# Kernel tuning notes

Hardware: AMD Instinct MI355X
Metric: run time of the kernel (lower is better)

Reference implementation:

```python
import jax, jax.numpy as jnp
import numpy as np

ALPHA = 0.3        # Keras LeakyReLU default negative_slope
NUM_STEPS = 16     # fixed-step Dormand-Prince (see notes)
DEPTH = 10
HID = 1024
LOOK = 30
BATCH = 16384


def _leaky(x):
    return jnp.where(x > 0, x, ALPHA * x)


def _mlp(y, W1, b1, W2, b2, W3, b3):
    # drift f(y): 30 -> 1024 -> 1024 -> 30, autonomous (t unused)
    h = _leaky(jnp.dot(y, W1) + b1)
    h = _leaky(jnp.dot(h, W2) + b2)
    return jnp.dot(h, W3) + b3


def _dopri5_step(y, h, params):
    f = lambda z: _mlp(z, *params)
    k1 = f(y)
    k2 = f(y + h * (1.0 / 5.0) * k1)
    k3 = f(y + h * (3.0 / 40.0 * k1 + 9.0 / 40.0 * k2))
    k4 = f(y + h * (44.0 / 45.0 * k1 - 56.0 / 15.0 * k2 + 32.0 / 9.0 * k3))
    k5 = f(y + h * (19372.0 / 6561.0 * k1 - 25360.0 / 2187.0 * k2
                    + 64448.0 / 6561.0 * k3 - 212.0 / 729.0 * k4))
    k6 = f(y + h * (9017.0 / 3168.0 * k1 - 355.0 / 33.0 * k2
                    + 46732.0 / 5247.0 * k3 + 49.0 / 176.0 * k4
                    - 5103.0 / 18656.0 * k5))
    # 5th-order solution (b row of the Dormand-Prince tableau)
    return y + h * (35.0 / 384.0 * k1 + 500.0 / 1113.0 * k3
                    + 125.0 / 192.0 * k4 - 2187.0 / 6784.0 * k5
                    + 11.0 / 84.0 * k6)


def _solve_block(y0, params):
    # integrate dy/dt = f(y) from t=0 to t=1 with fixed step h
    h = 1.0 / NUM_STEPS
    def step(y, _):
        return _dopri5_step(y, h, params), None
    y, _ = jax.lax.scan(step, y0, None, length=NUM_STEPS)
    return y


def setup_inputs() -> dict:
    key = jax.random.key(0)
    ks = jax.random.split(key, 9)
    y0 = jax.random.normal(ks[0], (BATCH, 1, LOOK), dtype=jnp.float32)
    s1 = 1.0 / np.sqrt(LOOK)
    s2 = 1.0 / np.sqrt(HID)
    W1 = jax.random.normal(ks[1], (DEPTH, LOOK, HID), dtype=jnp.float32) * s1
    b1 = jnp.zeros((DEPTH, HID), dtype=jnp.float32)
    W2 = jax.random.normal(ks[2], (DEPTH, HID, HID), dtype=jnp.float32) * s2
    b2 = jnp.zeros((DEPTH, HID), dtype=jnp.float32)
    W3 = jax.random.normal(ks[3], (DEPTH, HID, LOOK), dtype=jnp.float32) * s2
    b3 = jnp.zeros((DEPTH, LOOK), dtype=jnp.float32)
    Wf = jax.random.normal(ks[4], (LOOK, 1), dtype=jnp.float32) * s1
    bf = jnp.zeros((1,), dtype=jnp.float32)
    return {"y0": y0, "W1": W1, "b1": b1, "W2": W2, "b2": b2,
            "W3": W3, "b3": b3, "Wf": Wf, "bf": bf}


def reference(y0, W1, b1, W2, b2, W3, b3, Wf, bf):
    # sequentially apply DEPTH ODE blocks, each with its own drift MLP
    def block(y, p):
        return _solve_block(y, p), None
    y, _ = jax.lax.scan(block, y0, (W1, b1, W2, b2, W3, b3))
    # final readout Dense(output_dim=1)
    return jnp.dot(y, Wf) + bf  # (B, 1, 1)
```

## Files before the change

### kernel.cpp

```cpp
#include <hip/hip_runtime.h>

#define BATCH 16384
#define LOOK 30
#define HID 1024
#define DEPTH 10
#define NSTEPS 16
#define ALPHA 0.3f

typedef short bf16x8 __attribute__((ext_vector_type(8)));
typedef float f32x4 __attribute__((ext_vector_type(4)));

__device__ __forceinline__ float leaky(float x) { return x > 0.f ? x : ALPHA * x; }

__device__ __forceinline__ unsigned short f2bf(float x) {
  unsigned u = __builtin_bit_cast(unsigned, x);
  unsigned r = u + 0x7FFFu + ((u >> 16) & 1u);
  return (unsigned short)(r >> 16);
}
__device__ __forceinline__ float bf2f(unsigned short b) {
  return __builtin_bit_cast(float, (unsigned)b << 16);
}

#define GLD_LDS16(g, l)                                        \
  __builtin_amdgcn_global_load_lds(                            \
      (const __attribute__((address_space(1))) void*)(g),      \
      (__attribute__((address_space(3))) void*)(l), 16, 0, 0)

__global__ __launch_bounds__(256) void k_w2split(const float* __restrict__ W2d,
                                                 short* __restrict__ W2Th,
                                                 short* __restrict__ W2Tl) {
  __shared__ float t[64][65];
  const int kb = blockIdx.x * 64;
  const int nb = blockIdx.y * 64;
  for (int i = threadIdx.x; i < 4096; i += 256) {
    int r = i >> 6, c = i & 63;
    t[r][c] = W2d[(size_t)(kb + r) * HID + nb + c];
  }
  __syncthreads();
  for (int i = threadIdx.x; i < 4096; i += 256) {
    int r = i >> 6, c = i & 63;
    float v = t[c][r];
    unsigned short hi = f2bf(v);
    unsigned short lo = f2bf(v - bf2f(hi));
    W2Th[(size_t)(nb + r) * HID + kb + c] = (short)hi;
    W2Tl[(size_t)(nb + r) * HID + kb + c] = (short)lo;
  }
}

__global__ __launch_bounds__(256) void k_w1t(const float* __restrict__ W1d,
                                             short* __restrict__ W1Th,
                                             short* __restrict__ W1Tl) {
  const int idx = blockIdx.x * 256 + threadIdx.x;
  if (idx >= 1024 * 32) return;
  const int n = idx >> 5, k = idx & 31;
  float v = (k < LOOK) ? W1d[(size_t)k * HID + n] : 0.f;
  unsigned short hi = f2bf(v);
  unsigned short lo = f2bf(v - bf2f(hi));
  W1Th[idx] = (short)hi;
  W1Tl[idx] = (short)lo;
}

__global__ __launch_bounds__(256) void k_w3t(const float* __restrict__ W3d,
                                             short* __restrict__ W3Th,
                                             short* __restrict__ W3Tl) {
  const int idx = blockIdx.x * 256 + threadIdx.x;
  if (idx >= 32 * 1024) return;
  const int n = idx >> 10, k = idx & 1023;
  float v = (n < LOOK) ? W3d[(size_t)k * LOOK + n] : 0.f;
  unsigned short hi = f2bf(v);
  unsigned short lo = f2bf(v - bf2f(hi));
  W3Th[idx] = (short)hi;
  W3Tl[idx] = (short)lo;
}

__global__ __launch_bounds__(256) void k_zinit(const float* __restrict__ y0,
                                               short* __restrict__ zh,
                                               short* __restrict__ zl) {
  const int idx = blockIdx.x * 256 + threadIdx.x;
  if (idx >= BATCH * 32) return;
  const int r = idx >> 5, c = idx & 31;
  float v = (c < LOOK) ? y0[(size_t)r * LOOK + c] : 0.f;
  unsigned short hi = f2bf(v);
  unsigned short lo = f2bf(v - bf2f(hi));
  zh[idx] = (short)hi;
  zl[idx] = (short)lo;
}

__global__ __launch_bounds__(512, 2) void k_l1(
    const short* __restrict__ zh, const short* __restrict__ zl,
    const short* __restrict__ W1Th, const short* __restrict__ W1Tl,
    const float* __restrict__ b1d, short* __restrict__ H1h,
    short* __restrict__ H1l) {
  __shared__ short za[2][128 * 32];
  const int tid = threadIdx.x, lane = tid & 63, wave = tid >> 6;
  const int row0 = blockIdx.x * 128;
  const int n0 = blockIdx.y * 256;
  const int wm = wave >> 2, wn = wave & 3;
  const int r15 = lane & 15;
  const int bk = (lane >> 4) * 8;

  bf16x8 bh[4], bl[4];
#pragma unroll
  for (int nj = 0; nj < 4; ++nj) {
    const size_t bo = (size_t)(n0 + wn * 64 + nj * 16 + r15) * 32 + bk;
    bh[nj] = *(const bf16x8*)&W1Th[bo];
    bl[nj] = *(const bf16x8*)&W1Tl[bo];
  }

  GLD_LDS16((const char*)(zh + (size_t)row0 * 32) + tid * 16, &za[0][tid * 8]);
  GLD_LDS16((const char*)(zl + (size_t)row0 * 32) + tid * 16, &za[1][tid * 8]);
  __syncthreads();

  bf16x8 ah[4], al[4];
#pragma unroll
  for (int mi = 0; mi < 4; ++mi) {
    const int ao = (wm * 64 + mi * 16 + r15) * 32 + bk;
    ah[mi] = *(const bf16x8*)&za[0][ao];
    al[mi] = *(const bf16x8*)&za[1][ao];
  }

  f32x4 acc[4][4];
#pragma unroll
  for (int i = 0; i < 4; ++i)
#pragma unroll
    for (int j = 0; j < 4; ++j) acc[i][j] = (f32x4){0.f, 0.f, 0.f, 0.f};

#pragma unroll
  for (int mi = 0; mi < 4; ++mi)
#pragma unroll
    for (int nj = 0; nj < 4; ++nj) {
      acc[mi][nj] = __builtin_amdgcn_mfma_f32_16x16x32_bf16(ah[mi], bh[nj],
                                                            acc[mi][nj], 0, 0, 0);
      acc[mi][nj] = __builtin_amdgcn_mfma_f32_16x16x32_bf16(ah[mi], bl[nj],
                                                            acc[mi][nj], 0, 0, 0);
      acc[mi][nj] = __builtin_amdgcn_mfma_f32_16x16x32_bf16(al[mi], bh[nj],
                                                            acc[mi][nj], 0, 0, 0);
    }

  const int crow = (lane >> 4) * 4;
#pragma unroll
  for (int nj = 0; nj < 4; ++nj) {
    const int col = n0 + wn * 64 + nj * 16 + r15;
    const float bias = b1d[col];
#pragma unroll
    for (int mi = 0; mi < 4; ++mi) {
      const int rb = row0 + wm * 64 + mi * 16 + crow;
#pragma unroll
      for (int r = 0; r < 4; ++r) {
        float v = leaky(acc[mi][nj][r] + bias);
        unsigned short hi = f2bf(v);
        unsigned short lo = f2bf(v - bf2f(hi));
        const size_t o = (size_t)(rb + r) * HID + col;
        H1h[o] = (short)hi;
        H1l[o] = (short)lo;
      }
    }
  }
}

__global__ __launch_bounds__(512, 2) void k_mid(
    const short* __restrict__ H1h, const short* __restrict__ H1l,
    const short* __restrict__ W2Th, const short* __restrict__ W2Tl,
    const float* __restrict__ b2d, short* __restrict__ H2h,
    short* __restrict__ H2l) {
  __shared__ char lds[131072];

  const int tid = threadIdx.x;
  const int lane = tid & 63;
  const int wave = tid >> 6;

  const int bid = blockIdx.x;
  const int wg = (bid & 7) * 32 + (bid >> 3);
  const int mb = wg >> 2, nb = wg & 3;
  const int row0 = mb * 256;
  const int n0 = nb * 256;
  const int wm = wave >> 2;
  const int wnb = wave & 3;

  const int l3 = lane >> 3;
  const int l7 = lane & 7;
  const int s = l7 ^ l3;
  const char* hsrc;
  const char* lsrc;
  int rbase;
  if (wave < 4) {
    hsrc = (const char*)H1h;
    lsrc = (const char*)H1l;
    rbase = row0;
  } else {
    hsrc = (const char*)W2Th;
    lsrc = (const char*)W2Tl;
    rbase = n0;
  }
  const char* srcB[8];
#pragma unroll
  for (int i = 0; i < 8; ++i) {
    const int c = wave * 8 + i;
    const int rloc = (c & 31) * 8 + l3;
    const char* base = (s < 4) ? hsrc : lsrc;
    srcB[i] = base + (size_t)(rbase + rloc) * 2048 + (size_t)(s & 3) * 16;
  }
  const int dchunk0 = wave * 8 * 1024;

  int offA0, offA1, offB0, offB1;
  {
    const int r15 = lane & 15;
    const int kq = lane >> 4;
    const int pa0 = ((0 * 4 + kq) ^ l7) * 16;
    const int pa1 = ((1 * 4 + kq) ^ l7) * 16;
    offA0 = (wm * 128 + r15) * 128 + pa0;
    offA1 = (wm * 128 + r15) * 128 + pa1;
    offB0 = 32768 + (wnb * 64 + r15) * 128 + pa0;
    offB1 = 32768 + (wnb * 64 + r15) * 128 + pa1;
  }

  f32x4 acc[8][4];
#pragma unroll
  for (int i = 0; i < 8; ++i)
#pragma unroll
    for (int j = 0; j < 4; ++j) acc[i][j] = (f32x4){0.f, 0.f, 0.f, 0.f};

#define STAGE(buf, kb)                                                   \
  {                                                                      \
    _Pragma("unroll") for (int i = 0; i < 8; ++i) {                      \
      GLD_LDS16(srcB[i] + (kb), &lds[(buf)*65536 + dchunk0 + i * 1024]); \
    }                                                                    \
  }

  STAGE(0, 0);
  __syncthreads();

  int cur = 0;
  for (int t = 0; t < 32; ++t) {
    if (t < 31) STAGE(cur ^ 1, (t + 1) * 64);

    const char* buf = &lds[cur * 65536];
    bf16x8 bh[4], bl[4];
#pragma unroll
    for (int nj = 0; nj < 4; ++nj) {
      bh[nj] = *(const bf16x8*)(buf + offB0 + nj * 2048);
      bl[nj] = *(const bf16x8*)(buf + offB1 + nj * 2048);
    }
#pragma unroll
    for (int mi = 0; mi < 8; ++mi) {
      bf16x8 ah = *(const bf16x8*)(buf + offA0 + mi * 2048);
      bf16x8 al = *(const bf16x8*)(buf + offA1 + mi * 2048);
#pragma unroll
      for (int nj = 0; nj < 4; ++nj) {
        acc[mi][nj] =
            __builtin_amdgcn_mfma_f32_16x16x32_bf16(ah, bh[nj], acc[mi][nj], 0, 0, 0);
        acc[mi][nj] =
            __builtin_amdgcn_mfma_f32_16x16x32_bf16(ah, bl[nj], acc[mi][nj], 0, 0, 0);
        acc[mi][nj] =
            __builtin_amdgcn_mfma_f32_16x16x32_bf16(al, bh[nj], acc[mi][nj], 0, 0, 0);
      }
    }
    __syncthreads();
    cur ^= 1;
  }
#undef STAGE

  const int crow = (lane >> 4) * 4;
  const int ccol = lane & 15;
#pragma unroll
  for (int nj = 0; nj < 4; ++nj) {
    const int col = n0 + wnb * 64 + nj * 16 + ccol;
    const float bv = b2d[col];
#pragma unroll
    for (int mi = 0; mi < 8; ++mi) {
      const int rb = row0 + wm * 128 + mi * 16 + crow;
#pragma unroll
      for (int r = 0; r < 4; ++r) {
        float v = leaky(acc[mi][nj][r] + bv);
        unsigned short hi = f2bf(v);
        unsigned short lo = f2bf(v - bf2f(hi));
        const size_t o = (size_t)(rb + r) * HID + col;
        H2h[o] = (short)hi;
        H2l[o] = (short)lo;
      }
    }
  }
}

__global__ __launch_bounds__(256, 4) void k_l3(
    const short* __restrict__ H2h, const short* __restrict__ H2l,
    const short* __restrict__ W3Th, const short* __restrict__ W3Tl,
    const float* __restrict__ b3d, float* __restrict__ kout,
    const float* __restrict__ K0, const float* __restrict__ K1,
    const float* __restrict__ K2, const float* __restrict__ K3,
    const float* __restrict__ K4, float* __restrict__ y,
    short* __restrict__ zh, short* __restrict__ zl, int combine, float p1,
    float p2, float p3, float p4, float p5, float pc, float hb1, float hb2,
    float hb3, float hb4, float hb5, float hb6) {
  __shared__ short lds[2][4096];

  const int tid = threadIdx.x, lane = tid & 63, wave = tid >> 6;
  const int row0 = blockIdx.x * 32;
  const int wm = wave & 1, wn = wave >> 1;

  const int half = tid >> 7;
  const int idx = tid & 127;
  const int srow = idx >> 2;
  const int sd = idx & 3;
  const int slog = sd ^ ((srow >> 1) & 3);
  const short* Asrc = half ? H2l : H2h;
  const short* Bsrc = half ? W3Tl : W3Th;
  const char* aSrc = (const char*)(Asrc + (size_t)(row0 + srow) * HID) + slog * 16;
  const char* bSrc = (const char*)(Bsrc + (size_t)srow * HID) + slog * 16;
  short* aDst0 = &lds[0][half * 1024 + idx * 8];
  short* bDst0 = &lds[0][2048 + half * 1024 + idx * 8];
  short* aDst1 = &lds[1][half * 1024 + idx * 8];
  short* bDst1 = &lds[1][2048 + half * 1024 + idx * 8];

  const int r15 = lane & 15;
  const int kc = lane >> 4;
  const int aRow = wm * 16 + r15;
  const int bRow = wn * 16 + r15;
  const int aOff = aRow * 32 + (kc ^ ((aRow >> 1) & 3)) * 8;
  const int bOff = 2048 + bRow * 32 + (kc ^ ((bRow >> 1) & 3)) * 8;

  f32x4 acc = (f32x4){0.f, 0.f, 0.f, 0.f};

#define STAGE3(ad, bd, kb)          \
  {                                 \
    GLD_LDS16(aSrc + (kb), (ad));   \
    GLD_LDS16(bSrc + (kb), (bd));   \
  }

  STAGE3(aDst0, bDst0, 0);
  __syncthreads();

  for (int t = 0; t < 32; ++t) {
    const int cur = t & 1;
    if (t < 31) {
      if (cur == 0) STAGE3(aDst1, bDst1, (t + 1) * 64)
      else STAGE3(aDst0, bDst0, (t + 1) * 64)
    }
    const short* buf = lds[cur];
    bf16x8 ah = *(const bf16x8*)(buf + aOff);
    bf16x8 al = *(const bf16x8*)(buf + 1024 + aOff);
    bf16x8 bh = *(const bf16x8*)(buf + bOff);
    bf16x8 bl = *(const bf16x8*)(buf + 1024 + bOff);
    acc = __builtin_amdgcn_mfma_f32_16x16x32_bf16(ah, bh, acc, 0, 0, 0);
    acc = __builtin_amdgcn_mfma_f32_16x16x32_bf16(ah, bl, acc, 0, 0, 0);
    acc = __builtin_amdgcn_mfma_f32_16x16x32_bf16(al, bh, acc, 0, 0, 0);
    __syncthreads();
  }
#undef STAGE3

  const int c = wn * 16 + r15;
  const int rb = row0 + wm * 16 + (lane >> 4) * 4;
  const float bias = (c < LOOK) ? b3d[c] : 0.f;
#pragma unroll
  for (int r = 0; r < 4; ++r) {
    const int row = rb + r;
    const float kv = acc[r] + bias;
    float zv = 0.f;
    if (c < LOOK) {
      const size_t id = (size_t)row * LOOK + c;
      const float yv = y[id];
      if (combine) {
        float yn = yv + hb1 * K0[id] + hb2 * K1[id] + hb3 * K2[id] +
                   hb4 * K3[id] + hb5 * K4[id] + hb6 * kv;
        y[id] = yn;
        zv = yn;
      } else {
        kout[id] = kv;
        zv = yv + pc * kv;
        if (p1 != 0.f) zv += p1 * K0[id];
        if (p2 != 0.f) zv += p2 * K1[id];
        if (p3 != 0.f) zv += p3 * K2[id];
        if (p4 != 0.f) zv += p4 * K3[id];
        if (p5 != 0.f) zv += p5 * K4[id];
      }
    }
    unsigned short hi = f2bf(zv);
    unsigned short lo = f2bf(zv - bf2f(hi));
    const size_t zo = (size_t)row * 32 + c;
    zh[zo] = (short)hi;
    zl[zo] = (short)lo;
  }
}

__global__ __launch_bounds__(256) void k_readout(const float* __restrict__ y,
                                                 const float* __restrict__ Wf,
                                                 const float* __restrict__ bf,
                                                 float* __restrict__ out) {
  const int r = blockIdx.x * blockDim.x + threadIdx.x;
  if (r >= BATCH) return;
  float acc = bf[0];
#pragma unroll
  for (int c = 0; c < LOOK; ++c) acc += y[(size_t)r * LOOK + c] * Wf[c];
  out[r] = acc;
}

extern "C" void kernel_launch(void* const* d_in, const int* in_sizes, int n_in,
                              void* d_out, int out_size, void* d_ws,
                              size_t ws_size, hipStream_t stream) {
  const float* y0 = (const float*)d_in[0];
  const float* W1 = (const float*)d_in[1];
  const float* b1 = (const float*)d_in[2];
  const float* W2 = (const float*)d_in[3];
  const float* b2 = (const float*)d_in[4];
  const float* W3 = (const float*)d_in[5];
  const float* b3 = (const float*)d_in[6];
  const float* Wf = (const float*)d_in[7];
  const float* bf = (const float*)d_in[8];
  float* out = (float*)d_out;

  const size_t NY = (size_t)BATCH * LOOK;
  float* f = (float*)d_ws;
  float* y = f;
  float* kk[5];
  for (int i = 0; i < 5; ++i) kk[i] = f + NY * (1 + i);
  char* p = (char*)(f + NY * 6);
  short* zh = (short*)p; p += (size_t)BATCH * 32 * 2;
  short* zl = (short*)p; p += (size_t)BATCH * 32 * 2;
  short* H1h = (short*)p; p += (size_t)BATCH * HID * 2;
  short* H1l = (short*)p; p += (size_t)BATCH * HID * 2;
  short* H2h = (short*)p; p += (size_t)BATCH * HID * 2;
  short* H2l = (short*)p; p += (size_t)BATCH * HID * 2;
  short* W2Th = (short*)p; p += (size_t)HID * HID * 2;
  short* W2Tl = (short*)p; p += (size_t)HID * HID * 2;
  short* W1Th = (short*)p; p += (size_t)HID * 32 * 2;
  short* W1Tl = (short*)p; p += (size_t)HID * 32 * 2;
  short* W3Th = (short*)p; p += (size_t)32 * HID * 2;
  short* W3Tl = (short*)p;

  hipMemcpyAsync(y, y0, NY * sizeof(float), hipMemcpyDeviceToDevice, stream);
  k_zinit<<<dim3(BATCH * 32 / 256), 256, 0, stream>>>(y0, zh, zl);

  const double hh = 1.0 / 16.0;
  static const double A[6][5] = {
      {0, 0, 0, 0, 0},
      {1.0 / 5, 0, 0, 0, 0},
      {3.0 / 40, 9.0 / 40, 0, 0, 0},
      {44.0 / 45, -56.0 / 15, 32.0 / 9, 0, 0},
      {19372.0 / 6561, -25360.0 / 2187, 64448.0 / 6561, -212.0 / 729, 0},
      {9017.0 / 3168, -355.0 / 33, 46732.0 / 5247, 49.0 / 176,
       -5103.0 / 18656},
  };
  static const double Bb[6] = {35.0 / 384,  0,              500.0 / 1113,
                               125.0 / 192, -2187.0 / 6784, 11.0 / 84};

  const float hb1 = (float)(hh * Bb[0]);
  const float hb2 = (float)(hh * Bb[1]);
  const float hb3 = (float)(hh * Bb[2]);
  const float hb4 = (float)(hh * Bb[3]);
  const float hb5 = (float)(hh * Bb[4]);
  const float hb6 = (float)(hh * Bb[5]);

  for (int d = 0; d < DEPTH; ++d) {
    const float* W1d = W1 + (size_t)d * LOOK * HID;
    const float* b1d = b1 + (size_t)d * HID;
    const float* W2d = W2 + (size_t)d * HID * HID;
    const float* b2d = b2 + (size_t)d * HID;
    const float* W3d = W3 + (size_t)d * HID * LOOK;
    const float* b3d = b3 + (size_t)d * LOOK;

    k_w2split<<<dim3(16, 16), 256, 0, stream>>>(W2d, W2Th, W2Tl);
    k_w1t<<<dim3(128), 256, 0, stream>>>(W1d, W1Th, W1Tl);
    k_w3t<<<dim3(128), 256, 0, stream>>>(W3d, W3Th, W3Tl);

    for (int s = 0; s < NSTEPS; ++s) {
      for (int st = 0; st < 6; ++st) {
        float pv[5] = {0.f, 0.f, 0.f, 0.f, 0.f};
        float pc = 0.f;
        if (st < 5) {
          for (int jj = 0; jj < 5; ++jj)
            if (jj < st) pv[jj] = (float)(hh * A[st + 1][jj]);
          pc = (float)(hh * A[st + 1][st]);
        }
        k_l1<<<dim3(BATCH / 128, HID / 256), 512, 0, stream>>>(
            zh, zl, W1Th, W1Tl, b1d, H1h, H1l);
        k_mid<<<dim3(256), 512, 0, stream>>>(H1h, H1l, W2Th, W2Tl, b2d, H2h,
                                             H2l);
        const int comb = (st == 5) ? 1 : 0;
        float* kout = (st < 5) ? kk[st] : kk[0];
        k_l3<<<dim3(BATCH / 32), 256, 0, stream>>>(
            H2h, H2l, W3Th, W3Tl, b3d, kout, kk[0], kk[1], kk[2], kk[3],
            kk[4], y, zh, zl, comb, pv[0], pv[1], pv[2], pv[3], pv[4], pc,
            hb1, hb2, hb3, hb4, hb5, hb6);
      }
    }
  }

  k_readout<<<dim3(BATCH / 256), 256, 0, stream>>>(y, Wf, bf, out);
}
```

Baseline: 137.6 ms.

## Fuse first MLP layer into second-layer GEMM, computing H1 tiles on the fly

Removes the separate layer-1 kernel and its H1 hi/lo round trip through global memory. Each block now computes the 256x64 slice of H1 for every k-step with MFMA from the z inputs and W1, applies bias and leaky, splits the result into bf16 hi/lo and writes it straight into LDS for the W2 GEMM. Only the W2 tiles are double-buffered through global-to-LDS loads, synchronised with manual waitcnt and barriers plus setprio around the MFMA loop. The price is layer-1 work recomputed by each of the four N-blocks and extra per-iteration ALU and LDS-store work on the critical path.

Result: slower. 145.5 ms (+5.7%).

```diff
diff --git a/kernel.cpp b/kernel.cpp
--- a/kernel.cpp
+++ b/kernel.cpp
@@ -86,84 +86,13 @@
   zl[idx] = (short)lo;
 }
 
-__global__ __launch_bounds__(512, 2) void k_l1(
+__global__ __launch_bounds__(512, 2) void k_mid(
     const short* __restrict__ zh, const short* __restrict__ zl,
     const short* __restrict__ W1Th, const short* __restrict__ W1Tl,
-    const float* __restrict__ b1d, short* __restrict__ H1h,
-    short* __restrict__ H1l) {
-  __shared__ short za[2][128 * 32];
-  const int tid = threadIdx.x, lane = tid & 63, wave = tid >> 6;
-  const int row0 = blockIdx.x * 128;
-  const int n0 = blockIdx.y * 256;
-  const int wm = wave >> 2, wn = wave & 3;
-  const int r15 = lane & 15;
-  const int bk = (lane >> 4) * 8;
-
-  bf16x8 bh[4], bl[4];
-#pragma unroll
-  for (int nj = 0; nj < 4; ++nj) {
-    const size_t bo = (size_t)(n0 + wn * 64 + nj * 16 + r15) * 32 + bk;
-    bh[nj] = *(const bf16x8*)&W1Th[bo];
-    bl[nj] = *(const bf16x8*)&W1Tl[bo];
-  }
-
-  GLD_LDS16((const char*)(zh + (size_t)row0 * 32) + tid * 16, &za[0][tid * 8]);
-  GLD_LDS16((const char*)(zl + (size_t)row0 * 32) + tid * 16, &za[1][tid * 8]);
-  __syncthreads();
-
-  bf16x8 ah[4], al[4];
-#pragma unroll
-  for (int mi = 0; mi < 4; ++mi) {
-    const int ao = (wm * 64 + mi * 16 + r15) * 32 + bk;
-    ah[mi] = *(const bf16x8*)&za[0][ao];
-    al[mi] = *(const bf16x8*)&za[1][ao];
-  }
-
-  f32x4 acc[4][4];
-#pragma unroll
-  for (int i = 0; i < 4; ++i)
-#pragma unroll
-    for (int j = 0; j < 4; ++j) acc[i][j] = (f32x4){0.f, 0.f, 0.f, 0.f};
-
-#pragma unroll
-  for (int mi = 0; mi < 4; ++mi)
-#pragma unroll
-    for (int nj = 0; nj < 4; ++nj) {
-      acc[mi][nj] = __builtin_amdgcn_mfma_f32_16x16x32_bf16(ah[mi], bh[nj],
-                                                            acc[mi][nj], 0, 0, 0);
-      acc[mi][nj] = __builtin_amdgcn_mfma_f32_16x16x32_bf16(ah[mi], bl[nj],
-                                                            acc[mi][nj], 0, 0, 0);
-      acc[mi][nj] = __builtin_amdgcn_mfma_f32_16x16x32_bf16(al[mi], bh[nj],
-                                                            acc[mi][nj], 0, 0, 0);
-    }
-
-  const int crow = (lane >> 4) * 4;
-#pragma unroll
-  for (int nj = 0; nj < 4; ++nj) {
-    const int col = n0 + wn * 64 + nj * 16 + r15;
-    const float bias = b1d[col];
-#pragma unroll
-    for (int mi = 0; mi < 4; ++mi) {
-      const int rb = row0 + wm * 64 + mi * 16 + crow;
-#pragma unroll
-      for (int r = 0; r < 4; ++r) {
-        float v = leaky(acc[mi][nj][r] + bias);
-        unsigned short hi = f2bf(v);
-        unsigned short lo = f2bf(v - bf2f(hi));
-        const size_t o = (size_t)(rb + r) * HID + col;
-        H1h[o] = (short)hi;
-        H1l[o] = (short)lo;
-      }
-    }
-  }
-}
-
-__global__ __launch_bounds__(512, 2) void k_mid(
-    const short* __restrict__ H1h, const short* __restrict__ H1l,
-    const short* __restrict__ W2Th, const short* __restrict__ W2Tl,
-    const float* __restrict__ b2d, short* __restrict__ H2h,
-    short* __restrict__ H2l) {
-  __shared__ char lds[131072];
+    const float* __restrict__ b1d, const short* __restrict__ W2Th,
+    const short* __restrict__ W2Tl, const float* __restrict__ b2d,
+    short* __restrict__ H2h, short* __restrict__ H2l) {
+  __shared__ char lds[98304];
 
   const int tid = threadIdx.x;
   const int lane = tid & 63;
@@ -176,43 +105,34 @@
   const int n0 = nb * 256;
   const int wm = wave >> 2;
   const int wnb = wave & 3;
-
+  const int r15 = lane & 15;
+  const int kq = lane >> 4;
+  const int l7 = lane & 7;
   const int l3 = lane >> 3;
-  const int l7 = lane & 7;
-  const int s = l7 ^ l3;
-  const char* hsrc;
-  const char* lsrc;
-  int rbase;
-  if (wave < 4) {
-    hsrc = (const char*)H1h;
-    lsrc = (const char*)H1l;
-    rbase = row0;
-  } else {
-    hsrc = (const char*)W2Th;
-    lsrc = (const char*)W2Tl;
-    rbase = n0;
-  }
-  const char* srcB[8];
-#pragma unroll
-  for (int i = 0; i < 8; ++i) {
-    const int c = wave * 8 + i;
-    const int rloc = (c & 31) * 8 + l3;
-    const char* base = (s < 4) ? hsrc : lsrc;
-    srcB[i] = base + (size_t)(rbase + rloc) * 2048 + (size_t)(s & 3) * 16;
-  }
-  const int dchunk0 = wave * 8 * 1024;
-
-  int offA0, offA1, offB0, offB1;
+
+  const char* srcB[4];
   {
-    const int r15 = lane & 15;
-    const int kq = lane >> 4;
-    const int pa0 = ((0 * 4 + kq) ^ l7) * 16;
-    const int pa1 = ((1 * 4 + kq) ^ l7) * 16;
-    offA0 = (wm * 128 + r15) * 128 + pa0;
-    offA1 = (wm * 128 + r15) * 128 + pa1;
-    offB0 = 32768 + (wnb * 64 + r15) * 128 + pa0;
-    offB1 = 32768 + (wnb * 64 + r15) * 128 + pa1;
-  }
+    const int s = l7 ^ l3;
+    const char* base = (s < 4) ? (const char*)W2Th : (const char*)W2Tl;
+#pragma unroll
+    for (int i = 0; i < 4; ++i) {
+      const int c = wave * 4 + i;
+      srcB[i] = base + (size_t)(n0 + c * 8 + l3) * 2048 + (size_t)(s & 3) * 16;
+    }
+  }
+
+  bf16x8 zf[2][2];
+#pragma unroll
+  for (int rt = 0; rt < 2; ++rt) {
+    const size_t zo = (size_t)(row0 + wave * 32 + rt * 16 + r15) * 32 + kq * 8;
+    zf[rt][0] = *(const bf16x8*)&zh[zo];
+    zf[rt][1] = *(const bf16x8*)&zl[zo];
+  }
+
+  const int offA0 = (wm * 128 + r15) * 128 + ((0 + kq) ^ l7) * 16;
+  const int offA1 = (wm * 128 + r15) * 128 + ((4 + kq) ^ l7) * 16;
+  const int offB0 = (wnb * 64 + r15) * 128 + ((0 + kq) ^ l7) * 16;
+  const int offB1 = (wnb * 64 + r15) * 128 + ((4 + kq) ^ l7) * 16;
 
   f32x4 acc[8][4];
 #pragma unroll
@@ -220,31 +140,87 @@
 #pragma unroll
     for (int j = 0; j < 4; ++j) acc[i][j] = (f32x4){0.f, 0.f, 0.f, 0.f};
 
-#define STAGE(buf, kb)                                                   \
-  {                                                                      \
-    _Pragma("unroll") for (int i = 0; i < 8; ++i) {                      \
-      GLD_LDS16(srcB[i] + (kb), &lds[(buf)*65536 + dchunk0 + i * 1024]); \
-    }                                                                    \
-  }
-
-  STAGE(0, 0);
-  __syncthreads();
-
-  int cur = 0;
+#pragma unroll
+  for (int i = 0; i < 4; ++i)
+    GLD_LDS16(srcB[i], &lds[32768 + (wave * 4 + i) * 1024]);
+
   for (int t = 0; t < 32; ++t) {
-    if (t < 31) STAGE(cur ^ 1, (t + 1) * 64);
-
-    const char* buf = &lds[cur * 65536];
+    bf16x8 w1[2][2];
+    float4 b1v[2];
+#pragma unroll
+    for (int kt = 0; kt < 2; ++kt) {
+      const size_t wo = (size_t)(t * 32 + kt * 16 + r15) * 32 + kq * 8;
+      w1[kt][0] = *(const bf16x8*)&W1Th[wo];
+      w1[kt][1] = *(const bf16x8*)&W1Tl[wo];
+      b1v[kt] = *(const float4*)&b1d[t * 32 + kt * 16 + kq * 4];
+    }
+
+    if (t < 31) {
+      const int kb = (t + 1) * 64;
+      char* dst = &lds[32768 + ((t + 1) & 1) * 32768];
+#pragma unroll
+      for (int i = 0; i < 4; ++i)
+        GLD_LDS16(srcB[i] + kb, dst + (wave * 4 + i) * 1024);
+    }
+
+    f32x4 h1a[2][2];
+#pragma unroll
+    for (int kt = 0; kt < 2; ++kt)
+#pragma unroll
+      for (int rt = 0; rt < 2; ++rt) {
+        f32x4 a = (f32x4){0.f, 0.f, 0.f, 0.f};
+        a = __builtin_amdgcn_mfma_f32_16x16x32_bf16(w1[kt][0], zf[rt][0], a, 0, 0, 0);
+        a = __builtin_amdgcn_mfma_f32_16x16x32_bf16(w1[kt][1], zf[rt][0], a, 0, 0, 0);
+        a = __builtin_amdgcn_mfma_f32_16x16x32_bf16(w1[kt][0], zf[rt][1], a, 0, 0, 0);
+        h1a[kt][rt] = a;
+      }
+
+#pragma unroll
+    for (int kt = 0; kt < 2; ++kt)
+#pragma unroll
+      for (int rt = 0; rt < 2; ++rt) {
+        unsigned short hs[4], ls[4];
+#pragma unroll
+        for (int r = 0; r < 4; ++r) {
+          float v = leaky(h1a[kt][rt][r] + b1v[kt][r]);
+          hs[r] = f2bf(v);
+          ls[r] = f2bf(v - bf2f(hs[r]));
+        }
+        const int row = wave * 32 + rt * 16 + r15;
+        const int bb = row * 128 + (kq & 1) * 8;
+        const int so = kt * 2 + (kq >> 1);
+        const int sh = ((0 + so) ^ l7) * 16;
+        const int sl = ((4 + so) ^ l7) * 16;
+        uint2 hp, lp;
+        hp.x = (unsigned)hs[0] | ((unsigned)hs[1] << 16);
+        hp.y = (unsigned)hs[2] | ((unsigned)hs[3] << 16);
+        lp.x = (unsigned)ls[0] | ((unsigned)ls[1] << 16);
+        lp.y = (unsigned)ls[2] | ((unsigned)ls[3] << 16);
+        *(uint2*)&lds[bb + sh] = hp;
+        *(uint2*)&lds[bb + sl] = lp;
+      }
+
+    __builtin_amdgcn_sched_barrier(0);
+    if (t < 31) {
+      asm volatile("s_waitcnt vmcnt(4) lgkmcnt(0)" ::: "memory");
+    } else {
+      asm volatile("s_waitcnt vmcnt(0) lgkmcnt(0)" ::: "memory");
+    }
+    __builtin_amdgcn_sched_barrier(0);
+    __builtin_amdgcn_s_barrier();
+
+    const char* bufB = &lds[32768 + (t & 1) * 32768];
     bf16x8 bh[4], bl[4];
 #pragma unroll
     for (int nj = 0; nj < 4; ++nj) {
-      bh[nj] = *(const bf16x8*)(buf + offB0 + nj * 2048);
-      bl[nj] = *(const bf16x8*)(buf + offB1 + nj * 2048);
-    }
+      bh[nj] = *(const bf16x8*)(bufB + offB0 + nj * 2048);
+      bl[nj] = *(const bf16x8*)(bufB + offB1 + nj * 2048);
+    }
+    __builtin_amdgcn_s_setprio(1);
 #pragma unroll
     for (int mi = 0; mi < 8; ++mi) {
-      bf16x8 ah = *(const bf16x8*)(buf + offA0 + mi * 2048);
-      bf16x8 al = *(const bf16x8*)(buf + offA1 + mi * 2048);
+      bf16x8 ah = *(const bf16x8*)(lds + offA0 + mi * 2048);
+      bf16x8 al = *(const bf16x8*)(lds + offA1 + mi * 2048);
 #pragma unroll
       for (int nj = 0; nj < 4; ++nj) {
         acc[mi][nj] =
@@ -255,16 +231,16 @@
             __builtin_amdgcn_mfma_f32_16x16x32_bf16(al, bh[nj], acc[mi][nj], 0, 0, 0);
       }
     }
-    __syncthreads();
-    cur ^= 1;
-  }
-#undef STAGE
+    __builtin_amdgcn_s_setprio(0);
+
+    __builtin_amdgcn_sched_barrier(0);
+    __builtin_amdgcn_s_barrier();
+  }
 
   const int crow = (lane >> 4) * 4;
-  const int ccol = lane & 15;
 #pragma unroll
   for (int nj = 0; nj < 4; ++nj) {
-    const int col = n0 + wnb * 64 + nj * 16 + ccol;
+    const int col = n0 + wnb * 64 + nj * 16 + r15;
     const float bv = b2d[col];
 #pragma unroll
     for (int mi = 0; mi < 8; ++mi) {
@@ -416,8 +392,6 @@
   char* p = (char*)(f + NY * 6);
   short* zh = (short*)p; p += (size_t)BATCH * 32 * 2;
   short* zl = (short*)p; p += (size_t)BATCH * 32 * 2;
-  short* H1h = (short*)p; p += (size_t)BATCH * HID * 2;
-  short* H1l = (short*)p; p += (size_t)BATCH * HID * 2;
   short* H2h = (short*)p; p += (size_t)BATCH * HID * 2;
   short* H2l = (short*)p; p += (size_t)BATCH * HID * 2;
   short* W2Th = (short*)p; p += (size_t)HID * HID * 2;
@@ -471,10 +445,8 @@
             if (jj < st) pv[jj] = (float)(hh * A[st + 1][jj]);
           pc = (float)(hh * A[st + 1][st]);
         }
-        k_l1<<<dim3(BATCH / 128, HID / 256), 512, 0, stream>>>(
-            zh, zl, W1Th, W1Tl, b1d, H1h, H1l);
-        k_mid<<<dim3(256), 512, 0, stream>>>(H1h, H1l, W2Th, W2Tl, b2d, H2h,
-                                             H2l);
+        k_mid<<<dim3(256), 512, 0, stream>>>(zh, zl, W1Th, W1Tl, b1d, W2Th,
+                                             W2Tl, b2d, H2h, H2l);
         const int comb = (st == 5) ? 1 : 0;
         float* kout = (st < 5) ? kk[st] : kk[0];
         k_l3<<<dim3(BATCH / 32), 256, 0, stream>>>(
```

## Hand-schedule MFMA pipeline in k_mid and deepen k_l3 prefetch ring

Applied to the files above, without the earlier changes.

In k_mid, LDS fragment reads are split into two halves, each followed by its MFMA block. Explicit sched_barriers, waitcnts and s_setprio raise priority around the MFMA clusters, and the next tile's global-to-LDS loads are issued after the first fragment reads. In k_l3, the double buffer becomes a 4-slot ring with prefetch distance 2 and partial vmcnt waits, so more loads stay in flight. The aim is better overlap of memory and MFMA, at the cost of fragile manual scheduling and extra LDS in k_l3.

Result: slower. 140.8 ms (+2.3%).

```diff
diff --git a/kernel.cpp b/kernel.cpp
--- a/kernel.cpp
+++ b/kernel.cpp
@@ -25,6 +25,24 @@
   __builtin_amdgcn_global_load_lds(                            \
       (const __attribute__((address_space(1))) void*)(g),      \
       (__attribute__((address_space(3))) void*)(l), 16, 0, 0)
+
+#define SBAR()                               \
+  {                                          \
+    __builtin_amdgcn_sched_barrier(0);       \
+    __builtin_amdgcn_s_barrier();            \
+  }
+#define WAIT_LGKM0()                                          \
+  {                                                           \
+    __builtin_amdgcn_sched_barrier(0);                        \
+    asm volatile("s_waitcnt lgkmcnt(0)" ::: "memory");        \
+    __builtin_amdgcn_sched_barrier(0);                        \
+  }
+#define WAIT_VM(n)                                            \
+  {                                                           \
+    __builtin_amdgcn_sched_barrier(0);                        \
+    asm volatile("s_waitcnt vmcnt(" #n ")" ::: "memory");     \
+    __builtin_amdgcn_sched_barrier(0);                        \
+  }
 
 __global__ __launch_bounds__(256) void k_w2split(const float* __restrict__ W2d,
                                                  short* __restrict__ W2Th,
@@ -176,43 +194,40 @@
   const int n0 = nb * 256;
   const int wm = wave >> 2;
   const int wnb = wave & 3;
-
+  const int r15 = lane & 15;
+  const int kq = lane >> 4;
+  const int l7 = lane & 7;
   const int l3 = lane >> 3;
-  const int l7 = lane & 7;
-  const int s = l7 ^ l3;
-  const char* hsrc;
-  const char* lsrc;
-  int rbase;
-  if (wave < 4) {
-    hsrc = (const char*)H1h;
-    lsrc = (const char*)H1l;
-    rbase = row0;
-  } else {
-    hsrc = (const char*)W2Th;
-    lsrc = (const char*)W2Tl;
-    rbase = n0;
-  }
+
   const char* srcB[8];
-#pragma unroll
-  for (int i = 0; i < 8; ++i) {
-    const int c = wave * 8 + i;
-    const int rloc = (c & 31) * 8 + l3;
+  {
+    const int s = l7 ^ l3;
+    const char* hsrc;
+    const char* lsrc;
+    int rbase;
+    if (wave < 4) {
+      hsrc = (const char*)H1h;
+      lsrc = (const char*)H1l;
+      rbase = row0;
+    } else {
+      hsrc = (const char*)W2Th;
+      lsrc = (const char*)W2Tl;
+      rbase = n0;
+    }
     const char* base = (s < 4) ? hsrc : lsrc;
-    srcB[i] = base + (size_t)(rbase + rloc) * 2048 + (size_t)(s & 3) * 16;
-  }
-  const int dchunk0 = wave * 8 * 1024;
-
-  int offA0, offA1, offB0, offB1;
-  {
-    const int r15 = lane & 15;
-    const int kq = lane >> 4;
-    const int pa0 = ((0 * 4 + kq) ^ l7) * 16;
-    const int pa1 = ((1 * 4 + kq) ^ l7) * 16;
-    offA0 = (wm * 128 + r15) * 128 + pa0;
-    offA1 = (wm * 128 + r15) * 128 + pa1;
-    offB0 = 32768 + (wnb * 64 + r15) * 128 + pa0;
-    offB1 = 32768 + (wnb * 64 + r15) * 128 + pa1;
-  }
+#pragma unroll
+    for (int i = 0; i < 8; ++i) {
+      const int c = wave * 8 + i;
+      const int rloc = (c & 31) * 8 + l3;
+      srcB[i] = base + (size_t)(rbase + rloc) * 2048 + (size_t)(s & 3) * 16;
+    }
+  }
+  const int dchunk0 = wave * 8192;
+
+  const int offA0 = (wm * 128 + r15) * 128 + ((0 + kq) ^ l7) * 16;
+  const int offA1 = (wm * 128 + r15) * 128 + ((4 + kq) ^ l7) * 16;
+  const int offB0 = 32768 + (wnb * 64 + r15) * 128 + ((0 + kq) ^ l7) * 16;
+  const int offB1 = 32768 + (wnb * 64 + r15) * 128 + ((4 + kq) ^ l7) * 16;
 
   f32x4 acc[8][4];
 #pragma unroll
@@ -220,61 +235,96 @@
 #pragma unroll
     for (int j = 0; j < 4; ++j) acc[i][j] = (f32x4){0.f, 0.f, 0.f, 0.f};
 
-#define STAGE(buf, kb)                                                   \
-  {                                                                      \
-    _Pragma("unroll") for (int i = 0; i < 8; ++i) {                      \
-      GLD_LDS16(srcB[i] + (kb), &lds[(buf)*65536 + dchunk0 + i * 1024]); \
-    }                                                                    \
-  }
-
-  STAGE(0, 0);
-  __syncthreads();
-
-  int cur = 0;
-  for (int t = 0; t < 32; ++t) {
-    if (t < 31) STAGE(cur ^ 1, (t + 1) * 64);
-
-    const char* buf = &lds[cur * 65536];
-    bf16x8 bh[4], bl[4];
+#define STAGE4(bufbase, kb, h)                                             \
+  {                                                                        \
+    _Pragma("unroll") for (int i_ = 0; i_ < 4; ++i_) {                     \
+      GLD_LDS16(srcB[(h)*4 + i_] + (kb),                                   \
+                &lds[(bufbase) + dchunk0 + ((h)*4 + i_) * 1024]);          \
+    }                                                                      \
+  }
+
+  STAGE4(0, 0, 0);
+  STAGE4(0, 0, 1);
+  WAIT_VM(0);
+  SBAR();
+
+  for (int tt = 0; tt < 32; ++tt) {
+    const int rb = (tt & 1) * 65536;
+    const int wb = ((tt + 1) & 1) * 65536;
+    const int kb = (tt + 1) * 64;
+
+    bf16x8 bh[4], bl[4], ah[4], al[4];
+
 #pragma unroll
     for (int nj = 0; nj < 4; ++nj) {
-      bh[nj] = *(const bf16x8*)(buf + offB0 + nj * 2048);
-      bl[nj] = *(const bf16x8*)(buf + offB1 + nj * 2048);
-    }
+      bh[nj] = *(const bf16x8*)(lds + rb + offB0 + nj * 2048);
+      bl[nj] = *(const bf16x8*)(lds + rb + offB1 + nj * 2048);
+    }
+#pragma unroll
+    for (int q = 0; q < 4; ++q) {
+      ah[q] = *(const bf16x8*)(lds + rb + offA0 + q * 2048);
+      al[q] = *(const bf16x8*)(lds + rb + offA1 + q * 2048);
+    }
+    if (tt < 31) {
+      STAGE4(wb, kb, 0);
+      STAGE4(wb, kb, 1);
+    }
+    SBAR();
+    WAIT_LGKM0();
+    __builtin_amdgcn_s_setprio(1);
+#pragma unroll
+    for (int q = 0; q < 4; ++q)
+#pragma unroll
+      for (int nj = 0; nj < 4; ++nj) {
+        acc[q][nj] =
+            __builtin_amdgcn_mfma_f32_16x16x32_bf16(ah[q], bh[nj], acc[q][nj], 0, 0, 0);
+        acc[q][nj] =
+            __builtin_amdgcn_mfma_f32_16x16x32_bf16(ah[q], bl[nj], acc[q][nj], 0, 0, 0);
+        acc[q][nj] =
+            __builtin_amdgcn_mfma_f32_16x16x32_bf16(al[q], bh[nj], acc[q][nj], 0, 0, 0);
+      }
+    __builtin_amdgcn_s_setprio(0);
+    SBAR();
+
+#pragma unroll
+    for (int q = 0; q < 4; ++q) {
+      ah[q] = *(const bf16x8*)(lds + rb + offA0 + (4 + q) * 2048);
+      al[q] = *(const bf16x8*)(lds + rb + offA1 + (4 + q) * 2048);
+    }
+    SBAR();
+    WAIT_LGKM0();
+    __builtin_amdgcn_s_setprio(1);
+#pragma unroll
+    for (int q = 0; q < 4; ++q)
+#pragma unroll
+      for (int nj = 0; nj < 4; ++nj) {
+        acc[4 + q][nj] =
+            __builtin_amdgcn_mfma_f32_16x16x32_bf16(ah[q], bh[nj], acc[4 + q][nj], 0, 0, 0);
+        acc[4 + q][nj] =
+            __builtin_amdgcn_mfma_f32_16x16x32_bf16(ah[q], bl[nj], acc[4 + q][nj], 0, 0, 0);
+        acc[4 + q][nj] =
+            __builtin_amdgcn_mfma_f32_16x16x32_bf16(al[q], bh[nj], acc[4 + q][nj], 0, 0, 0);
+      }
+    __builtin_amdgcn_s_setprio(0);
+    WAIT_VM(0);
+    SBAR();
+  }
+#undef STAGE4
+
+  const int crow = (lane >> 4) * 4;
+#pragma unroll
+  for (int nj = 0; nj < 4; ++nj) {
+    const int col = n0 + wnb * 64 + nj * 16 + r15;
+    const float bv = b2d[col];
 #pragma unroll
     for (int mi = 0; mi < 8; ++mi) {
-      bf16x8 ah = *(const bf16x8*)(buf + offA0 + mi * 2048);
-      bf16x8 al = *(const bf16x8*)(buf + offA1 + mi * 2048);
-#pragma unroll
-      for (int nj = 0; nj < 4; ++nj) {
-        acc[mi][nj] =
-            __builtin_amdgcn_mfma_f32_16x16x32_bf16(ah, bh[nj], acc[mi][nj], 0, 0, 0);
-        acc[mi][nj] =
-            __builtin_amdgcn_mfma_f32_16x16x32_bf16(ah, bl[nj], acc[mi][nj], 0, 0, 0);
-        acc[mi][nj] =
-            __builtin_amdgcn_mfma_f32_16x16x32_bf16(al, bh[nj], acc[mi][nj], 0, 0, 0);
-      }
-    }
-    __syncthreads();
-    cur ^= 1;
-  }
-#undef STAGE
-
-  const int crow = (lane >> 4) * 4;
-  const int ccol = lane & 15;
-#pragma unroll
-  for (int nj = 0; nj < 4; ++nj) {
-    const int col = n0 + wnb * 64 + nj * 16 + ccol;
-    const float bv = b2d[col];
-#pragma unroll
-    for (int mi = 0; mi < 8; ++mi) {
-      const int rb = row0 + wm * 128 + mi * 16 + crow;
+      const int rbrow = row0 + wm * 128 + mi * 16 + crow;
 #pragma unroll
       for (int r = 0; r < 4; ++r) {
         float v = leaky(acc[mi][nj][r] + bv);
         unsigned short hi = f2bf(v);
         unsigned short lo = f2bf(v - bf2f(hi));
-        const size_t o = (size_t)(rb + r) * HID + col;
+        const size_t o = (size_t)(rbrow + r) * HID + col;
         H2h[o] = (short)hi;
         H2l[o] = (short)lo;
       }
@@ -292,7 +342,7 @@
     short* __restrict__ zh, short* __restrict__ zl, int combine, float p1,
     float p2, float p3, float p4, float p5, float pc, float hb1, float hb2,
     float hb3, float hb4, float hb5, float hb6) {
-  __shared__ short lds[2][4096];
+  __shared__ short lds[4][4096];
 
   const int tid = threadIdx.x, lane = tid & 63, wave = tid >> 6;
   const int row0 = blockIdx.x * 32;
@@ -307,10 +357,13 @@
   const short* Bsrc = half ? W3Tl : W3Th;
   const char* aSrc = (const char*)(Asrc + (size_t)(row0 + srow) * HID) + slog * 16;
   const char* bSrc = (const char*)(Bsrc + (size_t)srow * HID) + slog * 16;
-  short* aDst0 = &lds[0][half * 1024 + idx * 8];
-  short* bDst0 = &lds[0][2048 + half * 1024 + idx * 8];
-  short* aDst1 = &lds[1][half * 1024 + idx * 8];
-  short* bDst1 = &lds[1][2048 + half * 1024 + idx * 8];
+  short* aDst[4];
+  short* bDst[4];
+#pragma unroll
+  for (int s = 0; s < 4; ++s) {
+    aDst[s] = &lds[s][half * 1024 + idx * 8];
+    bDst[s] = &lds[s][2048 + half * 1024 + idx * 8];
+  }
 
   const int r15 = lane & 15;
   const int kc = lane >> 4;
@@ -321,22 +374,20 @@
 
   f32x4 acc = (f32x4){0.f, 0.f, 0.f, 0.f};
 
-#define STAGE3(ad, bd, kb)          \
-  {                                 \
-    GLD_LDS16(aSrc + (kb), (ad));   \
-    GLD_LDS16(bSrc + (kb), (bd));   \
-  }
-
-  STAGE3(aDst0, bDst0, 0);
-  __syncthreads();
+#define STG(s, kb)                        \
+  {                                       \
+    GLD_LDS16(aSrc + (kb), aDst[s]);      \
+    GLD_LDS16(bSrc + (kb), bDst[s]);      \
+  }
+
+  STG(0, 0);
+  STG(1, 64);
+  WAIT_VM(2);
+  SBAR();
 
   for (int t = 0; t < 32; ++t) {
-    const int cur = t & 1;
-    if (t < 31) {
-      if (cur == 0) STAGE3(aDst1, bDst1, (t + 1) * 64)
-      else STAGE3(aDst0, bDst0, (t + 1) * 64)
-    }
-    const short* buf = lds[cur];
+    if (t + 2 < 32) STG((t + 2) & 3, (t + 2) * 64);
+    const short* buf = lds[t & 3];
     bf16x8 ah = *(const bf16x8*)(buf + aOff);
     bf16x8 al = *(const bf16x8*)(buf + 1024 + aOff);
     bf16x8 bh = *(const bf16x8*)(buf + bOff);
@@ -344,16 +395,21 @@
     acc = __builtin_amdgcn_mfma_f32_16x16x32_bf16(ah, bh, acc, 0, 0, 0);
     acc = __builtin_amdgcn_mfma_f32_16x16x32_bf16(ah, bl, acc, 0, 0, 0);
     acc = __builtin_amdgcn_mfma_f32_16x16x32_bf16(al, bh, acc, 0, 0, 0);
-    __syncthreads();
-  }
-#undef STAGE3
+    if (t + 2 < 32) {
+      WAIT_VM(2);
+    } else {
+      WAIT_VM(0);
+    }
+    SBAR();
+  }
+#undef STG
 
   const int c = wn * 16 + r15;
-  const int rb = row0 + wm * 16 + (lane >> 4) * 4;
+  const int rbrow = row0 + wm * 16 + (lane >> 4) * 4;
   const float bias = (c < LOOK) ? b3d[c] : 0.f;
 #pragma unroll
   for (int r = 0; r < 4; ++r) {
-    const int row = rb + r;
+    const int row = rbrow + r;
     const float kv = acc[r] + bias;
     float zv = 0.f;
     if (c < LOOK) {
```

## Load W2 operand directly from global and quad-buffer activations with one barrier per step

Applied to the files above, without the earlier changes.

The hidden-layer GEMM kernel stops staging the weight (B) tile through LDS. Each wave now reads its B fragments directly from global memory. Only the activation (A) tile is staged, through a 4-deep LDS ring buffer with a prefetch distance of two iterations. Manual vmcnt waits with a single barrier per k-step replace the two __syncthreads, and s_setprio raises priority during the MFMA block. This halves LDS traffic and sync cost, but B is now reloaded per wave from global/L2 and those loads are exposed latency inside the loop.

New measurement: 163.6 ms. 18.9% more time.

```diff
diff --git a/kernel.cpp b/kernel.cpp
--- a/kernel.cpp
+++ b/kernel.cpp
@@ -176,42 +176,33 @@
   const int n0 = nb * 256;
   const int wm = wave >> 2;
   const int wnb = wave & 3;
-
+  const int r15 = lane & 15;
+  const int kq = lane >> 4;
+  const int l7 = lane & 7;
   const int l3 = lane >> 3;
-  const int l7 = lane & 7;
-  const int s = l7 ^ l3;
-  const char* hsrc;
-  const char* lsrc;
-  int rbase;
-  if (wave < 4) {
-    hsrc = (const char*)H1h;
-    lsrc = (const char*)H1l;
-    rbase = row0;
-  } else {
-    hsrc = (const char*)W2Th;
-    lsrc = (const char*)W2Tl;
-    rbase = n0;
-  }
-  const char* srcB[8];
-#pragma unroll
-  for (int i = 0; i < 8; ++i) {
-    const int c = wave * 8 + i;
-    const int rloc = (c & 31) * 8 + l3;
-    const char* base = (s < 4) ? hsrc : lsrc;
-    srcB[i] = base + (size_t)(rbase + rloc) * 2048 + (size_t)(s & 3) * 16;
-  }
-  const int dchunk0 = wave * 8 * 1024;
-
-  int offA0, offA1, offB0, offB1;
+
+  const char* srcA[4];
   {
-    const int r15 = lane & 15;
-    const int kq = lane >> 4;
-    const int pa0 = ((0 * 4 + kq) ^ l7) * 16;
-    const int pa1 = ((1 * 4 + kq) ^ l7) * 16;
-    offA0 = (wm * 128 + r15) * 128 + pa0;
-    offA1 = (wm * 128 + r15) * 128 + pa1;
-    offB0 = 32768 + (wnb * 64 + r15) * 128 + pa0;
-    offB1 = 32768 + (wnb * 64 + r15) * 128 + pa1;
+    const int s = l7 ^ l3;
+    const char* base = (s < 4) ? (const char*)H1h : (const char*)H1l;
+#pragma unroll
+    for (int i = 0; i < 4; ++i) {
+      const int c = wave * 4 + i;
+      srcA[i] = base + (size_t)(row0 + c * 8 + l3) * 2048 + (size_t)(s & 3) * 16;
+    }
+  }
+  const int dchunk0 = wave * 4096;
+
+  const int offA0 = (wm * 128 + r15) * 128 + ((0 + kq) ^ l7) * 16;
+  const int offA1 = (wm * 128 + r15) * 128 + ((4 + kq) ^ l7) * 16;
+
+  const short* bColH[4];
+  const short* bColL[4];
+#pragma unroll
+  for (int nj = 0; nj < 4; ++nj) {
+    const int col = n0 + wnb * 64 + nj * 16 + r15;
+    bColH[nj] = W2Th + (size_t)col * 1024 + kq * 8;
+    bColL[nj] = W2Tl + (size_t)col * 1024 + kq * 8;
   }
 
   f32x4 acc[8][4];
@@ -220,31 +211,44 @@
 #pragma unroll
     for (int j = 0; j < 4; ++j) acc[i][j] = (f32x4){0.f, 0.f, 0.f, 0.f};
 
-#define STAGE(buf, kb)                                                   \
-  {                                                                      \
-    _Pragma("unroll") for (int i = 0; i < 8; ++i) {                      \
-      GLD_LDS16(srcB[i] + (kb), &lds[(buf)*65536 + dchunk0 + i * 1024]); \
-    }                                                                    \
-  }
-
-  STAGE(0, 0);
-  __syncthreads();
-
-  int cur = 0;
+#define ISSUE_A(t_)                                                        \
+  {                                                                        \
+    _Pragma("unroll") for (int i_ = 0; i_ < 4; ++i_) {                     \
+      GLD_LDS16(srcA[i_] + (size_t)(t_) * 64,                              \
+                &lds[((t_) & 3) * 32768 + dchunk0 + i_ * 1024]);           \
+    }                                                                      \
+  }
+
+  ISSUE_A(0);
+  ISSUE_A(1);
+
   for (int t = 0; t < 32; ++t) {
-    if (t < 31) STAGE(cur ^ 1, (t + 1) * 64);
-
-    const char* buf = &lds[cur * 65536];
+    __builtin_amdgcn_sched_barrier(0);
+    if (t < 31) {
+      asm volatile("s_waitcnt vmcnt(4)" ::: "memory");
+    } else {
+      asm volatile("s_waitcnt vmcnt(0)" ::: "memory");
+    }
+    __builtin_amdgcn_sched_barrier(0);
+    __builtin_amdgcn_s_barrier();
+    __builtin_amdgcn_sched_barrier(0);
+
+    if (t < 30) ISSUE_A(t + 2);
+    __builtin_amdgcn_sched_barrier(0);
+
     bf16x8 bh[4], bl[4];
 #pragma unroll
     for (int nj = 0; nj < 4; ++nj) {
-      bh[nj] = *(const bf16x8*)(buf + offB0 + nj * 2048);
-      bl[nj] = *(const bf16x8*)(buf + offB1 + nj * 2048);
-    }
+      bh[nj] = *(const bf16x8*)(bColH[nj] + t * 32);
+      bl[nj] = *(const bf16x8*)(bColL[nj] + t * 32);
+    }
+
+    const char* abuf = &lds[(t & 3) * 32768];
+    __builtin_amdgcn_s_setprio(1);
 #pragma unroll
     for (int mi = 0; mi < 8; ++mi) {
-      bf16x8 ah = *(const bf16x8*)(buf + offA0 + mi * 2048);
-      bf16x8 al = *(const bf16x8*)(buf + offA1 + mi * 2048);
+      bf16x8 ah = *(const bf16x8*)(abuf + offA0 + mi * 2048);
+      bf16x8 al = *(const bf16x8*)(abuf + offA1 + mi * 2048);
 #pragma unroll
       for (int nj = 0; nj < 4; ++nj) {
         acc[mi][nj] =
@@ -255,16 +259,14 @@
             __builtin_amdgcn_mfma_f32_16x16x32_bf16(al, bh[nj], acc[mi][nj], 0, 0, 0);
       }
     }
-    __syncthreads();
-    cur ^= 1;
-  }
-#undef STAGE
+    __builtin_amdgcn_s_setprio(0);
+  }
+#undef ISSUE_A
 
   const int crow = (lane >> 4) * 4;
-  const int ccol = lane & 15;
 #pragma unroll
   for (int nj = 0; nj < 4; ++nj) {
-    const int col = n0 + wnb * 64 + nj * 16 + ccol;
+    const int col = n0 + wnb * 64 + nj * 16 + r15;
     const float bv = b2d[col];
 #pragma unroll
     for (int mi = 0; mi < 8; ++mi) {
```
